# Optimization experiments

Hardware: AMD Instinct MI355X
Metric: run time of the kernel (lower is better)

Reference implementation:

```python
import jax, jax.numpy as jnp
import numpy as np

B, L, D, H = 8, 1024, 512, 8  # L must equal len_ for the skew trick
DH = D // H


def setup_inputs() -> dict:
    key = jax.random.key(0)
    ks = jax.random.split(key, 6)
    s = 0.02
    return {
        "x": jax.random.normal(ks[0], (B, L, D), dtype=jnp.float32),
        "Wq": jax.random.normal(ks[1], (D, D), dtype=jnp.float32) * s,
        "Wk": jax.random.normal(ks[2], (D, D), dtype=jnp.float32) * s,
        "Wv": jax.random.normal(ks[3], (D, D), dtype=jnp.float32) * s,
        "We": jax.random.normal(ks[4], (L, DH), dtype=jnp.float32) * s,  # e_projection weight: (len_, d_head)
        "Wo": jax.random.normal(ks[5], (D, D), dtype=jnp.float32) * s,
        "bo": jnp.zeros((D,), dtype=jnp.float32),
        "unused": 0,
    }


def reference(x, Wq, Wk, Wv, We, Wo, bo, unused):
    Bx, Lx, Dx = x.shape
    q = (x @ Wq.T).reshape(Bx, Lx, H, DH)  # blhd
    k = (x @ Wk.T).reshape(Bx, Lx, H, DH)
    v = (x @ Wv.T).reshape(Bx, Lx, H, DH)

    # relative-position logits: e_projection(q) then permute -> (B, H, L, len_)
    qe = jnp.einsum('blhd,ed->bhle', q, We)

    # 'skew' trick: reflect-pad right by L-1, zero-pad (right 1, bottom L-1),
    # reshape (B,H,2L-1,2L) -> (B,H,2L,2L-1), slice [:L, L-1:] -> (B,H,L,L)
    qe = jnp.pad(qe, ((0, 0), (0, 0), (0, 0), (0, Lx - 1)), mode='reflect')
    qe = jnp.pad(qe, ((0, 0), (0, 0), (0, Lx - 1), (0, 1)))
    qe = qe.reshape(Bx, H, 2 * Lx, 2 * Lx - 1)
    s_rel = qe[:, :, :Lx, Lx - 1:]

    scale = 1.0 / jnp.sqrt(jnp.asarray(DH, dtype=x.dtype))
    scores = jnp.einsum('blhd,bshd->bhls', q, k)
    A = jax.nn.softmax(scale * (scores + s_rel), axis=-1)
    V = jnp.einsum('bhls,bshd->blhd', A, v).reshape(Bx, Lx, Dx)
    return V @ Wo.T + bo
```

## Files before the change

### kernel.cpp

```cpp
#include <hip/hip_runtime.h>

#define Lc 1024
#define Dc 512
#define Hc 8
#define DHc 64

typedef __attribute__((ext_vector_type(8))) short bf16x8;
typedef __attribute__((ext_vector_type(4))) float f32x4;

typedef __attribute__((address_space(1))) const unsigned int guint;
typedef __attribute__((address_space(3))) unsigned int luint;

__device__ __forceinline__ void gload_lds16(const void* g, void* l) {
    __builtin_amdgcn_global_load_lds((guint*)g, (luint*)l, 16, 0, 0);
}

__device__ __forceinline__ unsigned short f2bf(float f) {
    unsigned u = __float_as_uint(f);
    u += 0x7fffu + ((u >> 16) & 1u);
    return (unsigned short)(u >> 16);
}
__device__ __forceinline__ unsigned pk2(float a, float b) {
    return (unsigned)f2bf(a) | ((unsigned)f2bf(b) << 16);
}
__device__ __forceinline__ float bf2f(unsigned short s) { return __uint_as_float(((unsigned)s) << 16); }

__global__ void cvt_all_kernel(
    const float* __restrict__ x,  const float* __restrict__ Wq,
    const float* __restrict__ Wk, const float* __restrict__ Wv,
    const float* __restrict__ Wo, const float* __restrict__ We,
    unsigned short* __restrict__ xb,  unsigned short* __restrict__ wqb,
    unsigned short* __restrict__ wkb, unsigned short* __restrict__ wvb,
    unsigned short* __restrict__ wob, unsigned short* __restrict__ wet)
{
    int bid = blockIdx.x;
    const float* src; unsigned short* dst; size_t base;
    if      (bid < 4096) { src = x;  dst = xb;  base = (size_t)bid * 1024; }
    else if (bid < 4352) { src = Wq; dst = wqb; base = (size_t)(bid-4096) * 1024; }
    else if (bid < 4608) { src = Wk; dst = wkb; base = (size_t)(bid-4352) * 1024; }
    else if (bid < 4864) { src = Wv; dst = wvb; base = (size_t)(bid-4608) * 1024; }
    else if (bid < 5120) { src = Wo; dst = wob; base = (size_t)(bid-4864) * 1024; }
    else                 { src = We; dst = wet; base = (size_t)(bid-5120) * 1024; }
    size_t i = base + (size_t)threadIdx.x * 4;
    float4 a = *(const float4*)&src[i];
    *(uint2*)&dst[i] = make_uint2(pk2(a.x, a.y), pk2(a.z, a.w));
}

__global__ __launch_bounds__(256, 3) void proj_mfma_kernel(
    const unsigned short* __restrict__ xb,
    const unsigned short* __restrict__ wq, const unsigned short* __restrict__ wk,
    const unsigned short* __restrict__ wv,
    unsigned short* __restrict__ qo, unsigned short* __restrict__ ko,
    unsigned short* __restrict__ vtg, float qscale)
{
    const unsigned short* W;
    if (blockIdx.z == 0)      W = wq;
    else if (blockIdx.z == 1) W = wk;
    else                      W = wv;

    __shared__ unsigned short smem[128 * 136];
    unsigned short* As = smem;
    unsigned short* Bs = smem + 8192;

    const int t = threadIdx.x;
    const int lane = t & 63, w = t >> 6;
    const int lq = lane >> 4, ln = lane & 15;
    const int m0 = blockIdx.y * 128, n0 = blockIdx.x * 128;
    const int wm = (w & 1) * 64, wn = (w >> 1) * 64;
    const int srow = t >> 3;
    const int lsg  = ((t & 7) ^ ((t >> 3) & 7)) * 8;
    const int key  = ln & 7;

    f32x4 acc[4][4];
    #pragma unroll
    for (int i = 0; i < 4; i++)
        #pragma unroll
        for (int j = 0; j < 4; j++) acc[i][j] = (f32x4){0.f,0.f,0.f,0.f};

    for (int c0 = 0; c0 < 512; c0 += 64) {
        __syncthreads();
        #pragma unroll
        for (int g = 0; g < 4; g++) {
            gload_lds16(&xb[(size_t)(m0 + 32*g + srow) * 512 + c0 + lsg], &As[(32*g + srow)*64 + (t&7)*8]);
            gload_lds16(&W [(size_t)(n0 + 32*g + srow) * 512 + c0 + lsg], &Bs[(32*g + srow)*64 + (t&7)*8]);
        }
        __syncthreads();

        #pragma unroll
        for (int kk = 0; kk < 2; kk++) {
            bf16x8 af[4], bf[4];
            #pragma unroll
            for (int i = 0; i < 4; i++)
                af[i] = *(bf16x8*)&As[(wm + 16*i + ln)*64 + ((kk*4 + lq) ^ key)*8];
            #pragma unroll
            for (int j = 0; j < 4; j++)
                bf[j] = *(bf16x8*)&Bs[(wn + 16*j + ln)*64 + ((kk*4 + lq) ^ key)*8];
            #pragma unroll
            for (int i = 0; i < 4; i++)
                #pragma unroll
                for (int j = 0; j < 4; j++)
                    acc[i][j] = __builtin_amdgcn_mfma_f32_16x16x32_bf16(af[i], bf[j], acc[i][j], 0, 0, 0);
        }
    }

    if (blockIdx.z < 2) {
        unsigned short* out = (blockIdx.z == 0) ? qo : ko;
        const float osc = (blockIdx.z == 0) ? qscale : 1.0f;
        #pragma unroll
        for (int i = 0; i < 4; i++) {
            #pragma unroll
            for (int r = 0; r < 4; r++) {
                int m = m0 + wm + 16*i + 4*lq + r;
                int b = m >> 10, l = m & 1023;
                #pragma unroll
                for (int j = 0; j < 4; j++) {
                    int n = n0 + wn + 16*j + ln;
                    int h = n >> 6, dh = n & 63;
                    out[((size_t)((b*Hc + h)*Lc + l))*DHc + dh] = f2bf(acc[i][j][r] * osc);
                }
            }
        }
    } else {
        __syncthreads();
        unsigned short* Ts = smem;
        #pragma unroll
        for (int i = 0; i < 4; i++) {
            int mlb = wm + 16*i + 4*lq;
            #pragma unroll
            for (int j = 0; j < 4; j++) {
                int nl = wn + 16*j + ln;
                *(uint2*)&Ts[nl*136 + mlb] = make_uint2(pk2(acc[i][j][0], acc[i][j][1]),
                                                        pk2(acc[i][j][2], acc[i][j][3]));
            }
        }
        __syncthreads();
        const int b = m0 >> 10, l0m = m0 & 1023;
        const int nl = t >> 1, seg = (t & 1) * 64;
        const int ng = n0 + nl, h = ng >> 6, dh = ng & 63;
        unsigned short* dst = vtg + (((size_t)(b*Hc + h))*DHc + dh)*Lc + l0m + seg;
        #pragma unroll
        for (int u = 0; u < 8; u++)
            *(uint4*)&dst[8*u] = *(uint4*)&Ts[nl*136 + seg + 8*u];
    }
}

__global__ __launch_bounds__(256, 3) void out_mfma_kernel(
    const unsigned short* __restrict__ A, const unsigned short* __restrict__ W,
    const float* __restrict__ bias, float* __restrict__ out)
{
    __shared__ unsigned short As[128 * 64];
    __shared__ unsigned short Bs[128 * 64];

    const int t = threadIdx.x;
    const int lane = t & 63, w = t >> 6;
    const int lq = lane >> 4, ln = lane & 15;
    const int m0 = blockIdx.y * 128, n0 = blockIdx.x * 128;
    const int wm = (w & 1) * 64, wn = (w >> 1) * 64;
    const int srow = t >> 3;
    const int lsg  = ((t & 7) ^ ((t >> 3) & 7)) * 8;
    const int key  = ln & 7;

    f32x4 acc[4][4];
    #pragma unroll
    for (int i = 0; i < 4; i++)
        #pragma unroll
        for (int j = 0; j < 4; j++) acc[i][j] = (f32x4){0.f,0.f,0.f,0.f};

    for (int c0 = 0; c0 < 512; c0 += 64) {
        __syncthreads();
        #pragma unroll
        for (int g = 0; g < 4; g++) {
            gload_lds16(&A[(size_t)(m0 + 32*g + srow) * 512 + c0 + lsg], &As[(32*g + srow)*64 + (t&7)*8]);
            gload_lds16(&W[(size_t)(n0 + 32*g + srow) * 512 + c0 + lsg], &Bs[(32*g + srow)*64 + (t&7)*8]);
        }
        __syncthreads();

        #pragma unroll
        for (int kk = 0; kk < 2; kk++) {
            bf16x8 af[4], bf[4];
            #pragma unroll
            for (int i = 0; i < 4; i++)
                af[i] = *(bf16x8*)&As[(wm + 16*i + ln)*64 + ((kk*4 + lq) ^ key)*8];
            #pragma unroll
            for (int j = 0; j < 4; j++)
                bf[j] = *(bf16x8*)&Bs[(wn + 16*j + ln)*64 + ((kk*4 + lq) ^ key)*8];
            #pragma unroll
            for (int i = 0; i < 4; i++)
                #pragma unroll
                for (int j = 0; j < 4; j++)
                    acc[i][j] = __builtin_amdgcn_mfma_f32_16x16x32_bf16(af[i], bf[j], acc[i][j], 0, 0, 0);
        }
    }

    float bb[4];
    #pragma unroll
    for (int j = 0; j < 4; j++) bb[j] = bias[n0 + wn + 16*j + ln];

    #pragma unroll
    for (int i = 0; i < 4; i++) {
        #pragma unroll
        for (int r = 0; r < 4; r++) {
            int m = m0 + wm + 16*i + 4*lq + r;
            #pragma unroll
            for (int j = 0; j < 4; j++) {
                int n = n0 + wn + 16*j + ln;
                out[(size_t)m * Dc + n] = acc[i][j][r] + bb[j];
            }
        }
    }
}

__global__ __launch_bounds__(256, 3) void attn_v4_kernel(
    const unsigned short* __restrict__ q, const unsigned short* __restrict__ k,
    const unsigned short* __restrict__ vtg, const unsigned short* __restrict__ wet,
    unsigned short* __restrict__ attn)
{
    __shared__ unsigned short ksp [2 * 64 * 32];
    __shared__ unsigned short vtp [2 * 64 * 32];
    __shared__ unsigned short wesp[2 * 64 * 32];
    __shared__ unsigned short ps  [2 * 64 * 32];
    __shared__ unsigned short qes [2 * 64 * 68];

    const int t    = threadIdx.x;
    const int lane = t & 63, w = t >> 6;
    const int lq   = lane >> 4, ln = lane & 15;

    const int n   = blockIdx.x;
    const int xcd = n & 7, idx = n >> 3;
    const int bh  = xcd * 8 + (idx >> 4);
    const int l0  = (idx & 15) * 64;

    const unsigned short* qb  = q   + (size_t)bh * (Lc * DHc);
    const unsigned short* kb  = k   + (size_t)bh * (Lc * DHc);
    const unsigned short* vtb = vtg + (size_t)bh * (DHc * Lc);

    const int trow = t >> 2;
    const int sseg = ((t & 3) ^ ((t >> 4) & 3)) * 8;
    const int swz  = (ln >> 2) & 3;

    bf16x8 qa[2];
    #pragma unroll
    for (int kk = 0; kk < 2; kk++)
        qa[kk] = *(const bf16x8*)&qb[(size_t)(l0 + 16*w + ln)*64 + kk*32 + lq*8];

    const int pb0 = 15 - (l0 >> 6);
    gload_lds16(&wet[(size_t)(64*pb0 + trow)*64 +      sseg], &wesp[t*8]);
    gload_lds16(&wet[(size_t)(64*pb0 + trow)*64 + 32 + sseg], &wesp[2048 + t*8]);
    __syncthreads();
    {
        f32x4 qec[4];
        #pragma unroll
        for (int c = 0; c < 4; c++) qec[c] = (f32x4){0.f,0.f,0.f,0.f};
        #pragma unroll
        for (int kk = 0; kk < 2; kk++)
            #pragma unroll
            for (int c = 0; c < 4; c++) {
                bf16x8 bf = *(bf16x8*)&wesp[kk*2048 + (16*c + ln)*32 + (lq ^ swz)*8];
                qec[c] = __builtin_amdgcn_mfma_f32_16x16x32_bf16(qa[kk], bf, qec[c], 0, 0, 0);
            }
        const int slot = pb0 & 1;
        #pragma unroll
        for (int c = 0; c < 4; c++)
            *(uint2*)&qes[slot*4352 + (16*c + ln)*68 + 16*w + 4*lq] =
                make_uint2(pk2(qec[c][0], qec[c][1]), pk2(qec[c][2], qec[c][3]));
    }

    float lsum[4];
    f32x4 Ov[4];
    #pragma unroll
    for (int r = 0; r < 4; r++) lsum[r] = 0.f;
    #pragma unroll
    for (int c = 0; c < 4; c++) Ov[c] = (f32x4){0.f, 0.f, 0.f, 0.f};

    int pbOld = pb0 - 1;

    for (int s0 = 0; s0 < Lc; s0 += 64) {
        const int c0  = l0 - s0;
        const int ac0 = c0 < 0 ? -c0 : c0;
        const int pb  = (960 - ac0) >> 6;
        const int newp = (pb > pbOld) ? pb + 1 : pb;
        pbOld = pb;
        const int slot = newp & 1;

        __syncthreads();
        gload_lds16(&kb [(size_t)(s0 + trow)*64 +      sseg], &ksp [t*8]);
        gload_lds16(&kb [(size_t)(s0 + trow)*64 + 32 + sseg], &ksp [2048 + t*8]);
        gload_lds16(&vtb[(size_t)trow*1024 + s0 +      sseg], &vtp [t*8]);
        gload_lds16(&vtb[(size_t)trow*1024 + s0 + 32 + sseg], &vtp [2048 + t*8]);
        gload_lds16(&wet[(size_t)(64*newp + trow)*64 +      sseg], &wesp[t*8]);
        gload_lds16(&wet[(size_t)(64*newp + trow)*64 + 32 + sseg], &wesp[2048 + t*8]);
        __syncthreads();

        {
            f32x4 qec[4];
            #pragma unroll
            for (int c = 0; c < 4; c++) qec[c] = (f32x4){0.f,0.f,0.f,0.f};
            #pragma unroll
            for (int kk = 0; kk < 2; kk++)
                #pragma unroll
                for (int c = 0; c < 4; c++) {
                    bf16x8 bf = *(bf16x8*)&wesp[kk*2048 + (16*c + ln)*32 + (lq ^ swz)*8];
                    qec[c] = __builtin_amdgcn_mfma_f32_16x16x32_bf16(qa[kk], bf, qec[c], 0, 0, 0);
                }
            #pragma unroll
            for (int c = 0; c < 4; c++)
                *(uint2*)&qes[slot*4352 + (16*c + ln)*68 + 16*w + 4*lq] =
                    make_uint2(pk2(qec[c][0], qec[c][1]), pk2(qec[c][2], qec[c][3]));
        }

        f32x4 sc[4];
        #pragma unroll
        for (int c = 0; c < 4; c++) sc[c] = (f32x4){0.f,0.f,0.f,0.f};
        #pragma unroll
        for (int kk = 0; kk < 2; kk++)
            #pragma unroll
            for (int c = 0; c < 4; c++) {
                bf16x8 bfk = *(bf16x8*)&ksp[kk*2048 + (16*c + ln)*32 + (lq ^ swz)*8];
                sc[c] = __builtin_amdgcn_mfma_f32_16x16x32_bf16(qa[kk], bfk, sc[c], 0, 0, 0);
            }

        float p[4][4];
        #pragma unroll
        for (int r = 0; r < 4; r++) {
            const int lr = 16*w + 4*lq + r;
            const int dbase = c0 + lr - ln;
            float rs = 0.f;
            #pragma unroll
            for (int c = 0; c < 4; c++) {
                int d  = dbase - 16*c;
                int ad = d < 0 ? -d : d;
                int e  = 1023 - ad;
                float bias = bf2f(qes[((e >> 6) & 1)*4352 + (e & 63)*68 + lr]);
                float tv = sc[c][r] + bias;
                p[r][c] = __expf(tv);
                rs += p[r][c];
            }
            #pragma unroll
            for (int off = 1; off < 16; off <<= 1)
                rs += __shfl_xor(rs, off);
            lsum[r] += rs;
        }

        #pragma unroll
        for (int r = 0; r < 4; r++) {
            const int lr = 16*w + 4*lq + r;
            #pragma unroll
            for (int c = 0; c < 4; c++) {
                int seg = (((c & 1)*2 + (ln >> 3)) ^ lq);
                ps[(c >> 1)*2048 + lr*32 + seg*8 + (ln & 7)] = f2bf(p[r][c]);
            }
        }

        #pragma unroll
        for (int kk = 0; kk < 2; kk++) {
            bf16x8 pa = *(bf16x8*)&ps[kk*2048 + (16*w + ln)*32 + (lq ^ swz)*8];
            #pragma unroll
            for (int c = 0; c < 4; c++) {
                bf16x8 vf = *(bf16x8*)&vtp[kk*2048 + (16*c + ln)*32 + (lq ^ swz)*8];
                Ov[c] = __builtin_amdgcn_mfma_f32_16x16x32_bf16(pa, vf, Ov[c], 0, 0, 0);
            }
        }
    }

    const int b = bh >> 3, h = bh & 7;
    #pragma unroll
    for (int r = 0; r < 4; r++) {
        float inv = 1.f / lsum[r];
        int l = l0 + 16*w + 4*lq + r;
        #pragma unroll
        for (int c = 0; c < 4; c++)
            attn[((size_t)(b*Lc + l))*Dc + h*DHc + 16*c + ln] = f2bf(Ov[c][r] * inv);
    }
}

extern "C" void kernel_launch(void* const* d_in, const int* in_sizes, int n_in,
                              void* d_out, int out_size, void* d_ws, size_t ws_size,
                              hipStream_t stream)
{
    (void)in_sizes; (void)n_in; (void)out_size; (void)ws_size;
    const float* x  = (const float*)d_in[0];
    const float* Wq = (const float*)d_in[1];
    const float* Wk = (const float*)d_in[2];
    const float* Wv = (const float*)d_in[3];
    const float* We = (const float*)d_in[4];
    const float* Wo = (const float*)d_in[5];
    const float* bo = (const float*)d_in[6];

    const size_t NT = (size_t)8 * Hc * Lc * DHc;
    unsigned short* qw  = (unsigned short*)d_ws;
    unsigned short* kw  = qw  + NT;
    unsigned short* vtg = kw  + NT;
    unsigned short* xbf = vtg + NT;
    unsigned short* awb = xbf + NT;
    unsigned short* wqb = awb + NT;
    unsigned short* wkb = wqb + 262144;
    unsigned short* wvb = wkb + 262144;
    unsigned short* wob = wvb + 262144;
    unsigned short* wet = wob + 262144;

    cvt_all_kernel<<<5184, 256, 0, stream>>>(x, Wq, Wk, Wv, Wo, We,
                                             xbf, wqb, wkb, wvb, wob, wet);
    proj_mfma_kernel<<<dim3(4, 64, 3), 256, 0, stream>>>(xbf, wqb, wkb, wvb,
                                                         qw, kw, vtg, 0.125f);
    attn_v4_kernel<<<1024, 256, 0, stream>>>(qw, kw, vtg, wet, awb);
    out_mfma_kernel<<<dim3(4, 64), 256, 0, stream>>>(awb, wob, bo, (float*)d_out);
}
```

Measured before the change: 192.0 us.

## Fuse x bf16 conversion into projection, use exp2 and MFMA row sums

The projection kernel now reads fp32 x directly and converts it to bf16 while staging the tile into shared memory. This removes the separate full-tensor conversion pass and its workspace round trip, so the convert kernel only handles the weights. For Q and K the MFMA operands are swapped so each lane holds four consecutive head-dim values, which allows packed 8-byte stores instead of scalar ones. The attention kernel folds log2(e) into the Q scale so it can use exp2, packs probabilities to bf16 by truncation, and computes the softmax row sums with an MFMA against a ones vector instead of shuffle reductions. It also reshapes the relative-bias LDS buffer into one 128-row padded array; the tradeoffs are truncation rounding in P and non-async x loads in the projection.

```diff
diff --git a/kernel.cpp b/kernel.cpp
--- a/kernel.cpp
+++ b/kernel.cpp
@@ -20,34 +20,36 @@
     u += 0x7fffu + ((u >> 16) & 1u);
     return (unsigned short)(u >> 16);
 }
+__device__ __forceinline__ unsigned short f2bft(float f) {
+    return (unsigned short)(__float_as_uint(f) >> 16);
+}
 __device__ __forceinline__ unsigned pk2(float a, float b) {
     return (unsigned)f2bf(a) | ((unsigned)f2bf(b) << 16);
 }
 __device__ __forceinline__ float bf2f(unsigned short s) { return __uint_as_float(((unsigned)s) << 16); }
 
-__global__ void cvt_all_kernel(
-    const float* __restrict__ x,  const float* __restrict__ Wq,
-    const float* __restrict__ Wk, const float* __restrict__ Wv,
-    const float* __restrict__ Wo, const float* __restrict__ We,
-    unsigned short* __restrict__ xb,  unsigned short* __restrict__ wqb,
-    unsigned short* __restrict__ wkb, unsigned short* __restrict__ wvb,
-    unsigned short* __restrict__ wob, unsigned short* __restrict__ wet)
+__global__ void cvt_w_kernel(
+    const float* __restrict__ Wq, const float* __restrict__ Wk,
+    const float* __restrict__ Wv, const float* __restrict__ Wo,
+    const float* __restrict__ We,
+    unsigned short* __restrict__ wqb, unsigned short* __restrict__ wkb,
+    unsigned short* __restrict__ wvb, unsigned short* __restrict__ wob,
+    unsigned short* __restrict__ wet)
 {
     int bid = blockIdx.x;
     const float* src; unsigned short* dst; size_t base;
-    if      (bid < 4096) { src = x;  dst = xb;  base = (size_t)bid * 1024; }
-    else if (bid < 4352) { src = Wq; dst = wqb; base = (size_t)(bid-4096) * 1024; }
-    else if (bid < 4608) { src = Wk; dst = wkb; base = (size_t)(bid-4352) * 1024; }
-    else if (bid < 4864) { src = Wv; dst = wvb; base = (size_t)(bid-4608) * 1024; }
-    else if (bid < 5120) { src = Wo; dst = wob; base = (size_t)(bid-4864) * 1024; }
-    else                 { src = We; dst = wet; base = (size_t)(bid-5120) * 1024; }
+    if      (bid < 256)  { src = Wq; dst = wqb; base = (size_t)bid * 1024; }
+    else if (bid < 512)  { src = Wk; dst = wkb; base = (size_t)(bid-256) * 1024; }
+    else if (bid < 768)  { src = Wv; dst = wvb; base = (size_t)(bid-512) * 1024; }
+    else if (bid < 1024) { src = Wo; dst = wob; base = (size_t)(bid-768) * 1024; }
+    else                 { src = We; dst = wet; base = (size_t)(bid-1024) * 1024; }
     size_t i = base + (size_t)threadIdx.x * 4;
     float4 a = *(const float4*)&src[i];
     *(uint2*)&dst[i] = make_uint2(pk2(a.x, a.y), pk2(a.z, a.w));
 }
 
 __global__ __launch_bounds__(256, 3) void proj_mfma_kernel(
-    const unsigned short* __restrict__ xb,
+    const float* __restrict__ x,
     const unsigned short* __restrict__ wq, const unsigned short* __restrict__ wk,
     const unsigned short* __restrict__ wv,
     unsigned short* __restrict__ qo, unsigned short* __restrict__ ko,
@@ -69,6 +71,7 @@
     const int wm = (w & 1) * 64, wn = (w >> 1) * 64;
     const int srow = t >> 3;
     const int lsg  = ((t & 7) ^ ((t >> 3) & 7)) * 8;
+    const int arow = t >> 1, ahalf = (t & 1) * 4;
     const int key  = ln & 7;
 
     f32x4 acc[4][4];
@@ -80,9 +83,17 @@
     for (int c0 = 0; c0 < 512; c0 += 64) {
         __syncthreads();
         #pragma unroll
+        for (int g = 0; g < 4; g++)
+            gload_lds16(&W[(size_t)(n0 + 32*g + srow) * 512 + c0 + lsg], &Bs[(32*g + srow)*64 + (t&7)*8]);
+        #pragma unroll
         for (int g = 0; g < 4; g++) {
-            gload_lds16(&xb[(size_t)(m0 + 32*g + srow) * 512 + c0 + lsg], &As[(32*g + srow)*64 + (t&7)*8]);
-            gload_lds16(&W [(size_t)(n0 + 32*g + srow) * 512 + c0 + lsg], &Bs[(32*g + srow)*64 + (t&7)*8]);
+            int sl   = ahalf + g;
+            int pseg = sl ^ (arow & 7);
+            const float* s = &x[(size_t)(m0 + arow) * 512 + c0 + sl*8];
+            float4 a = *(const float4*)&s[0];
+            float4 b = *(const float4*)&s[4];
+            uint4 pv = make_uint4(pk2(a.x,a.y), pk2(a.z,a.w), pk2(b.x,b.y), pk2(b.z,b.w));
+            *(uint4*)&As[arow*64 + pseg*8] = pv;
         }
         __syncthreads();
 
@@ -95,11 +106,19 @@
             #pragma unroll
             for (int j = 0; j < 4; j++)
                 bf[j] = *(bf16x8*)&Bs[(wn + 16*j + ln)*64 + ((kk*4 + lq) ^ key)*8];
-            #pragma unroll
-            for (int i = 0; i < 4; i++)
+            if (blockIdx.z < 2) {
                 #pragma unroll
-                for (int j = 0; j < 4; j++)
-                    acc[i][j] = __builtin_amdgcn_mfma_f32_16x16x32_bf16(af[i], bf[j], acc[i][j], 0, 0, 0);
+                for (int i = 0; i < 4; i++)
+                    #pragma unroll
+                    for (int j = 0; j < 4; j++)
+                        acc[i][j] = __builtin_amdgcn_mfma_f32_16x16x32_bf16(bf[j], af[i], acc[i][j], 0, 0, 0);
+            } else {
+                #pragma unroll
+                for (int i = 0; i < 4; i++)
+                    #pragma unroll
+                    for (int j = 0; j < 4; j++)
+                        acc[i][j] = __builtin_amdgcn_mfma_f32_16x16x32_bf16(af[i], bf[j], acc[i][j], 0, 0, 0);
+            }
         }
     }
 
@@ -108,16 +127,15 @@
         const float osc = (blockIdx.z == 0) ? qscale : 1.0f;
         #pragma unroll
         for (int i = 0; i < 4; i++) {
-            #pragma unroll
-            for (int r = 0; r < 4; r++) {
-                int m = m0 + wm + 16*i + 4*lq + r;
-                int b = m >> 10, l = m & 1023;
-                #pragma unroll
-                for (int j = 0; j < 4; j++) {
-                    int n = n0 + wn + 16*j + ln;
-                    int h = n >> 6, dh = n & 63;
-                    out[((size_t)((b*Hc + h)*Lc + l))*DHc + dh] = f2bf(acc[i][j][r] * osc);
-                }
+            int m = m0 + wm + 16*i + ln;
+            int b = m >> 10, l = m & 1023;
+            #pragma unroll
+            for (int j = 0; j < 4; j++) {
+                int nb = n0 + wn + 16*j + 4*lq;
+                int h = nb >> 6, dh = nb & 63;
+                *(uint2*)&out[((size_t)((b*Hc + h)*Lc + l))*DHc + dh] =
+                    make_uint2(pk2(acc[i][j][0]*osc, acc[i][j][1]*osc),
+                               pk2(acc[i][j][2]*osc, acc[i][j][3]*osc));
             }
         }
     } else {
@@ -210,7 +228,7 @@
     }
 }
 
-__global__ __launch_bounds__(256, 3) void attn_v4_kernel(
+__global__ __launch_bounds__(256, 3) void attn_v5_kernel(
     const unsigned short* __restrict__ q, const unsigned short* __restrict__ k,
     const unsigned short* __restrict__ vtg, const unsigned short* __restrict__ wet,
     unsigned short* __restrict__ attn)
@@ -219,7 +237,7 @@
     __shared__ unsigned short vtp [2 * 64 * 32];
     __shared__ unsigned short wesp[2 * 64 * 32];
     __shared__ unsigned short ps  [2 * 64 * 32];
-    __shared__ unsigned short qes [2 * 64 * 68];
+    __shared__ unsigned short qes [128 * 70];
 
     const int t    = threadIdx.x;
     const int lane = t & 63, w = t >> 6;
@@ -237,6 +255,9 @@
     const int trow = t >> 2;
     const int sseg = ((t & 3) ^ ((t >> 4) & 3)) * 8;
     const int swz  = (ln >> 2) & 3;
+
+    const bf16x8 onesf = {(short)0x3F80,(short)0x3F80,(short)0x3F80,(short)0x3F80,
+                          (short)0x3F80,(short)0x3F80,(short)0x3F80,(short)0x3F80};
 
     bf16x8 qa[2];
     #pragma unroll
@@ -258,17 +279,15 @@
                 bf16x8 bf = *(bf16x8*)&wesp[kk*2048 + (16*c + ln)*32 + (lq ^ swz)*8];
                 qec[c] = __builtin_amdgcn_mfma_f32_16x16x32_bf16(qa[kk], bf, qec[c], 0, 0, 0);
             }
-        const int slot = pb0 & 1;
+        const int cb = (pb0 & 1) * 64;
         #pragma unroll
         for (int c = 0; c < 4; c++)
-            *(uint2*)&qes[slot*4352 + (16*c + ln)*68 + 16*w + 4*lq] =
+            *(uint2*)&qes[(cb + 16*c + ln)*70 + 16*w + 4*lq] =
                 make_uint2(pk2(qec[c][0], qec[c][1]), pk2(qec[c][2], qec[c][3]));
     }
 
-    float lsum[4];
+    f32x4 Lacc = (f32x4){0.f, 0.f, 0.f, 0.f};
     f32x4 Ov[4];
-    #pragma unroll
-    for (int r = 0; r < 4; r++) lsum[r] = 0.f;
     #pragma unroll
     for (int c = 0; c < 4; c++) Ov[c] = (f32x4){0.f, 0.f, 0.f, 0.f};
 
@@ -280,7 +299,7 @@
         const int pb  = (960 - ac0) >> 6;
         const int newp = (pb > pbOld) ? pb + 1 : pb;
         pbOld = pb;
-        const int slot = newp & 1;
+        const int cb = (newp & 1) * 64;
 
         __syncthreads();
         gload_lds16(&kb [(size_t)(s0 + trow)*64 +      sseg], &ksp [t*8]);
@@ -304,7 +323,7 @@
                 }
             #pragma unroll
             for (int c = 0; c < 4; c++)
-                *(uint2*)&qes[slot*4352 + (16*c + ln)*68 + 16*w + 4*lq] =
+                *(uint2*)&qes[(cb + 16*c + ln)*70 + 16*w + 4*lq] =
                     make_uint2(pk2(qec[c][0], qec[c][1]), pk2(qec[c][2], qec[c][3]));
         }
 
@@ -324,21 +343,14 @@
         for (int r = 0; r < 4; r++) {
             const int lr = 16*w + 4*lq + r;
             const int dbase = c0 + lr - ln;
-            float rs = 0.f;
             #pragma unroll
             for (int c = 0; c < 4; c++) {
                 int d  = dbase - 16*c;
                 int ad = d < 0 ? -d : d;
-                int e  = 1023 - ad;
-                float bias = bf2f(qes[((e >> 6) & 1)*4352 + (e & 63)*68 + lr]);
-                float tv = sc[c][r] + bias;
-                p[r][c] = __expf(tv);
-                rs += p[r][c];
-            }
-            #pragma unroll
-            for (int off = 1; off < 16; off <<= 1)
-                rs += __shfl_xor(rs, off);
-            lsum[r] += rs;
+                int m  = 1023 - ad;
+                float bias = bf2f(qes[(m & 127)*70 + lr]);
+                p[r][c] = __builtin_amdgcn_exp2f(sc[c][r] + bias);
+            }
         }
 
         #pragma unroll
@@ -347,13 +359,14 @@
             #pragma unroll
             for (int c = 0; c < 4; c++) {
                 int seg = (((c & 1)*2 + (ln >> 3)) ^ lq);
-                ps[(c >> 1)*2048 + lr*32 + seg*8 + (ln & 7)] = f2bf(p[r][c]);
+                ps[(c >> 1)*2048 + lr*32 + seg*8 + (ln & 7)] = f2bft(p[r][c]);
             }
         }
 
         #pragma unroll
         for (int kk = 0; kk < 2; kk++) {
             bf16x8 pa = *(bf16x8*)&ps[kk*2048 + (16*w + ln)*32 + (lq ^ swz)*8];
+            Lacc = __builtin_amdgcn_mfma_f32_16x16x32_bf16(pa, onesf, Lacc, 0, 0, 0);
             #pragma unroll
             for (int c = 0; c < 4; c++) {
                 bf16x8 vf = *(bf16x8*)&vtp[kk*2048 + (16*c + ln)*32 + (lq ^ swz)*8];
@@ -365,7 +378,7 @@
     const int b = bh >> 3, h = bh & 7;
     #pragma unroll
     for (int r = 0; r < 4; r++) {
-        float inv = 1.f / lsum[r];
+        float inv = 1.f / Lacc[r];
         int l = l0 + 16*w + 4*lq + r;
         #pragma unroll
         for (int c = 0; c < 4; c++)
@@ -390,18 +403,18 @@
     unsigned short* qw  = (unsigned short*)d_ws;
     unsigned short* kw  = qw  + NT;
     unsigned short* vtg = kw  + NT;
-    unsigned short* xbf = vtg + NT;
-    unsigned short* awb = xbf + NT;
+    unsigned short* awb = vtg + NT;
     unsigned short* wqb = awb + NT;
     unsigned short* wkb = wqb + 262144;
     unsigned short* wvb = wkb + 262144;
     unsigned short* wob = wvb + 262144;
     unsigned short* wet = wob + 262144;
 
-    cvt_all_kernel<<<5184, 256, 0, stream>>>(x, Wq, Wk, Wv, Wo, We,
-                                             xbf, wqb, wkb, wvb, wob, wet);
-    proj_mfma_kernel<<<dim3(4, 64, 3), 256, 0, stream>>>(xbf, wqb, wkb, wvb,
-                                                         qw, kw, vtg, 0.125f);
-    attn_v4_kernel<<<1024, 256, 0, stream>>>(qw, kw, vtg, wet, awb);
+    cvt_w_kernel<<<1088, 256, 0, stream>>>(Wq, Wk, Wv, Wo, We,
+                                           wqb, wkb, wvb, wob, wet);
+    proj_mfma_kernel<<<dim3(4, 64, 3), 256, 0, stream>>>(x, wqb, wkb, wvb,
+                                                         qw, kw, vtg,
+                                                         0.125f * 1.44269504089f);
+    attn_v5_kernel<<<1024, 256, 0, stream>>>(qw, kw, vtg, wet, awb);
     out_mfma_kernel<<<dim3(4, 64), 256, 0, stream>>>(awb, wob, bo, (float*)d_out);
 }
```

Result: slower. 222.1 us (+15.7%).
